# Kernel tuning notes

Hardware: AMD Instinct MI355X
Metric: run time of the kernel (lower is better)

Reference implementation:

```python
import jax, jax.numpy as jnp
import numpy as np

N = 16384
E = 524288
IN_DIM, H1, H2 = 256, 128, 64


def setup_inputs() -> dict:
    key = jax.random.key(0)
    ks = jax.random.split(key, 9)
    features = jax.random.normal(ks[0], (N, IN_DIM), dtype=jnp.float32)
    src = jax.random.randint(ks[1], (E,), 0, N, dtype=jnp.int32)
    dst = jax.random.randint(ks[2], (E,), 0, N, dtype=jnp.int32)
    s = 0.1
    W1 = jax.random.normal(ks[3], (IN_DIM, H1), dtype=jnp.float32) * s
    b1 = jnp.zeros((H1,), dtype=jnp.float32)
    W2 = jax.random.normal(ks[4], (H1, H1), dtype=jnp.float32) * s
    b2 = jnp.zeros((H1,), dtype=jnp.float32)
    W3 = jax.random.normal(ks[5], (H1, H2), dtype=jnp.float32) * s
    b3 = jnp.zeros((H2,), dtype=jnp.float32)
    return {"features": features, "src": src, "dst": dst,
            "W1": W1, "b1": b1, "W2": W2, "b2": b2, "W3": W3, "b3": b3}


def _degree_norms(src, dst):
    ones = jnp.ones(src.shape[0], dtype=jnp.float32)
    deg_out = jax.ops.segment_sum(ones, src, num_segments=N)
    deg_in = jax.ops.segment_sum(ones, dst, num_segments=N)
    # allow_zero_in_degree=True with norm='both': clamp degree to min 1
    norm_out = jax.lax.rsqrt(jnp.maximum(deg_out, 1.0))  # [N]
    norm_in = jax.lax.rsqrt(jnp.maximum(deg_in, 1.0))    # [N]
    return norm_out, norm_in


def _graph_conv(h, src, dst, norm_out, norm_in, W, b, relu):
    # DGL GraphConv, norm='both': D_in^{-1/2} A^T (D_out^{-1/2} h) W + b
    h = h * norm_out[:, None]
    msg = h[src]                                   # gather [E, d]
    agg = jax.ops.segment_sum(msg, dst, num_segments=N)  # scatter-add [N, d]
    out = agg * norm_in[:, None] @ W + b
    return jax.nn.relu(out) if relu else out


def reference(features, src, dst, W1, b1, W2, b2, W3, b3):
    norm_out, norm_in = _degree_norms(src, dst)
    h = _graph_conv(features, src, dst, norm_out, norm_in, W1, b1, True)
    h = _graph_conv(h, src, dst, norm_out, norm_in, W2, b2, True)
    z = _graph_conv(h, src, dst, norm_out, norm_in, W3, b3, False)  # [N, H2]
    adj_rec = jax.nn.sigmoid(z @ z.T)  # [N, N]
    return adj_rec, z
```

## Files before the change

kernel.cpp:

```cpp
#include <hip/hip_runtime.h>
#include <hip/hip_bf16.h>

#define NN 16384
#define EE 524288

constexpr int D0 = 256, D1 = 128, D2 = 64;

typedef __attribute__((ext_vector_type(8))) short short8;
typedef __attribute__((ext_vector_type(4))) float f32x4;

__device__ __forceinline__ float b2f(ushort u) {
  union { unsigned int i; float f; } x;
  x.i = ((unsigned int)u) << 16;
  return x.f;
}
__device__ __forceinline__ ushort f2b(float f) {
  __hip_bfloat16 h = __float2bfloat16(f);
  return *reinterpret_cast<ushort*>(&h);
}


__global__ __launch_bounds__(256) void count_deg_kernel(
    const int* __restrict__ src, const int* __restrict__ dst,
    int* __restrict__ deg_out, int* __restrict__ deg_in) {
  int e = blockIdx.x * 256 + threadIdx.x;
  if (e < EE) {
    atomicAdd(&deg_out[src[e]], 1);
    atomicAdd(&deg_in[dst[e]], 1);
  }
}

__global__ __launch_bounds__(256) void norm_kernel(
    const int* __restrict__ deg_out, const int* __restrict__ deg_in,
    float* __restrict__ norm_out, float* __restrict__ norm_in) {
  int i = blockIdx.x * 256 + threadIdx.x;
  if (i < NN) {
    norm_out[i] = rsqrtf(fmaxf((float)deg_out[i], 1.0f));
    norm_in[i]  = rsqrtf(fmaxf((float)deg_in[i], 1.0f));
  }
}

__global__ __launch_bounds__(256) void prefix_kernel(
    const int* __restrict__ deg_in, int* __restrict__ row_ptr,
    int* __restrict__ cursor) {
  __shared__ int part[256];
  int t = threadIdx.x;
  int base = t * 64;
  int s = 0;
  for (int j = 0; j < 64; ++j) s += deg_in[base + j];
  part[t] = s;
  __syncthreads();
  for (int off = 1; off < 256; off <<= 1) {
    int add = (t >= off) ? part[t - off] : 0;
    __syncthreads();
    part[t] += add;
    __syncthreads();
  }
  int run = (t == 0) ? 0 : part[t - 1];
  for (int j = 0; j < 64; ++j) {
    row_ptr[base + j] = run;
    cursor[base + j] = run;
    run += deg_in[base + j];
  }
  if (t == 255) row_ptr[NN] = run;
}

__global__ __launch_bounds__(256) void fill_csr_kernel(
    const int* __restrict__ src, const int* __restrict__ dst,
    int* __restrict__ cursor, int* __restrict__ csr_src) {
  int e = blockIdx.x * 256 + threadIdx.x;
  if (e < EE) {
    int pos = atomicAdd(&cursor[dst[e]], 1);
    csr_src[pos] = src[e];
  }
}


template<int DIN, int DOUT, int KC, bool OBF16>
__global__ __launch_bounds__(256) void gemm_kernel(
    const float* __restrict__ h, const float* __restrict__ W,
    const float* __restrict__ norm_out, float* __restrict__ tf,
    ushort* __restrict__ tb) {
  constexpr int W4 = DOUT / 4;
  constexpr int RG = 256 / W4;
  constexpr int RPT = 32 / RG;
  __shared__ float A[32][DIN];
  __shared__ float WC[KC][DOUT];
  int tid = threadIdx.x;
  int r0 = blockIdx.x * 32;
  constexpr int NF4 = 32 * DIN / 4;
  for (int q = tid; q < NF4; q += 256) {
    int r = q / (DIN / 4);
    int c = q % (DIN / 4);
    float4 x = *(const float4*)&h[(size_t)(r0 + r) * DIN + c * 4];
    float no = norm_out[r0 + r];
    x.x *= no; x.y *= no; x.z *= no; x.w *= no;
    *(float4*)&A[r][c * 4] = x;
  }
  int c4 = tid % W4;
  int rg = tid / W4;
  float4 acc[RPT];
#pragma unroll
  for (int j = 0; j < RPT; ++j) acc[j] = make_float4(0.f, 0.f, 0.f, 0.f);

  for (int kc = 0; kc < DIN / KC; ++kc) {
    __syncthreads();
#pragma unroll
    for (int q = 0; q < KC * W4 / 256; ++q)
      ((float4*)WC)[q * 256 + tid] =
          ((const float4*)W)[(size_t)kc * KC * W4 + q * 256 + tid];
    __syncthreads();
#pragma unroll 4
    for (int k2 = 0; k2 < KC; ++k2) {
      float4 w = *(const float4*)&WC[k2][c4 * 4];
#pragma unroll
      for (int j = 0; j < RPT; ++j) {
        float a = A[rg + j * RG][kc * KC + k2];
        acc[j].x += a * w.x; acc[j].y += a * w.y;
        acc[j].z += a * w.z; acc[j].w += a * w.w;
      }
    }
  }
#pragma unroll
  for (int j = 0; j < RPT; ++j) {
    size_t row = (size_t)(r0 + rg + j * RG);
    if (OBF16) {
      ushort4 o;
      o.x = f2b(acc[j].x); o.y = f2b(acc[j].y);
      o.z = f2b(acc[j].z); o.w = f2b(acc[j].w);
      *(ushort4*)&tb[row * DOUT + c4 * 4] = o;
    } else {
      *(float4*)&tf[row * DOUT + c4 * 4] = acc[j];
    }
  }
}


template<int DOUT, bool RELU>
__global__ __launch_bounds__(256) void gather_bf16_kernel(
    const ushort* __restrict__ t, const float* __restrict__ bias,
    const float* __restrict__ norm_in, const int* __restrict__ row_ptr,
    const int* __restrict__ csr, float* __restrict__ out) {
  constexpr int G8 = DOUT / 8;
  constexpr int S = 256 / G8;
  __shared__ float red[S][G8][8];
  int tid = threadIdx.x;
  int c8 = tid % G8, slot = tid / G8;
  int v = blockIdx.x;
  int k0 = row_ptr[v], k1 = row_ptr[v + 1];
  float a[8];
#pragma unroll
  for (int i = 0; i < 8; ++i) a[i] = 0.f;
  for (int k = k0 + slot; k < k1; k += S) {
    int s = csr[k];
    short8 m = *(const short8*)&t[(size_t)s * DOUT + c8 * 8];
#pragma unroll
    for (int i = 0; i < 8; ++i) a[i] += b2f((ushort)m[i]);
  }
#pragma unroll
  for (int i = 0; i < 8; ++i) red[slot][c8][i] = a[i];
  __syncthreads();
#pragma unroll
  for (int s = S / 2; s >= 1; s >>= 1) {
    if (slot < s) {
#pragma unroll
      for (int i = 0; i < 8; ++i) red[slot][c8][i] += red[slot + s][c8][i];
    }
    __syncthreads();
  }
  if (tid < G8) {
    float ni = norm_in[v];
    float o[8];
#pragma unroll
    for (int i = 0; i < 8; ++i) {
      o[i] = red[0][tid][i] * ni + bias[tid * 8 + i];
      if (RELU) o[i] = fmaxf(o[i], 0.f);
    }
    *(float4*)&out[(size_t)v * DOUT + tid * 8] = make_float4(o[0], o[1], o[2], o[3]);
    *(float4*)&out[(size_t)v * DOUT + tid * 8 + 4] = make_float4(o[4], o[5], o[6], o[7]);
  }
}


template<int DOUT, bool RELU>
__global__ __launch_bounds__(256) void gather_f32_kernel(
    const float* __restrict__ t, const float* __restrict__ bias,
    const float* __restrict__ norm_in, const int* __restrict__ row_ptr,
    const int* __restrict__ csr, float* __restrict__ out,
    ushort* __restrict__ zb) {
  constexpr int W4 = DOUT / 4;
  constexpr int S = 256 / W4;
  __shared__ float4 red[256];
  int tid = threadIdx.x;
  int c4 = tid % W4, slot = tid / W4;
  int v = blockIdx.x;
  int k0 = row_ptr[v], k1 = row_ptr[v + 1];
  float4 acc = make_float4(0.f, 0.f, 0.f, 0.f);
  for (int k = k0 + slot; k < k1; k += S) {
    int s = csr[k];
    float4 m = *(const float4*)&t[(size_t)s * DOUT + c4 * 4];
    acc.x += m.x; acc.y += m.y; acc.z += m.z; acc.w += m.w;
  }
  red[tid] = acc;
  __syncthreads();
  if (tid < W4) {
    float4 a = red[tid];
#pragma unroll
    for (int s = 1; s < S; ++s) {
      float4 b = red[s * W4 + tid];
      a.x += b.x; a.y += b.y; a.z += b.z; a.w += b.w;
    }
    float ni = norm_in[v];
    float4 b4 = *(const float4*)&bias[tid * 4];
    a.x = a.x * ni + b4.x; a.y = a.y * ni + b4.y;
    a.z = a.z * ni + b4.z; a.w = a.w * ni + b4.w;
    if (RELU) {
      a.x = fmaxf(a.x, 0.f); a.y = fmaxf(a.y, 0.f);
      a.z = fmaxf(a.z, 0.f); a.w = fmaxf(a.w, 0.f);
    }
    *(float4*)&out[(size_t)v * DOUT + tid * 4] = a;
    ushort4 ob;
    ob.x = f2b(a.x); ob.y = f2b(a.y); ob.z = f2b(a.z); ob.w = f2b(a.w);
    *(ushort4*)&zb[(size_t)v * DOUT + tid * 4] = ob;
  }
}


__global__ __launch_bounds__(256) void adj_mfma_kernel(
    const ushort* __restrict__ zb, float* __restrict__ C) {
  __shared__ ushort SMEM[2 * 128 * 64];
  ushort* ZR = SMEM;
  ushort* ZC = SMEM + 128 * 64;
  int t = threadIdx.x;
  int bx = blockIdx.x & 127, by = blockIdx.x >> 7;
  int row0 = by * 128, col0 = bx * 128;
  {
    int r = t >> 1;
    int ub = (t & 1) * 4;
    const float4* zr = (const float4*)(zb + (size_t)(row0 + r) * 64);
    const float4* zc = (const float4*)(zb + (size_t)(col0 + r) * 64);
    float4* LR = (float4*)ZR;
    float4* LC = (float4*)ZC;
#pragma unroll
    for (int u = 0; u < 4; ++u) {
      int sw = (ub + u) ^ (r & 7);
      LR[r * 8 + sw] = zr[ub + u];
      LC[r * 8 + sw] = zc[ub + u];
    }
  }
  __syncthreads();
  int l = t & 63, w = t >> 6;
  int wy = w >> 1, wx = w & 1;
  int lr = l & 15, lg = l >> 4;
  f32x4 acc[4][4];
#pragma unroll
  for (int i = 0; i < 4; ++i)
#pragma unroll
    for (int j = 0; j < 4; ++j) acc[i][j] = (f32x4){0.f, 0.f, 0.f, 0.f};

#pragma unroll
  for (int ks = 0; ks < 2; ++ks) {
    short8 af[4], bf_[4];
    int u = ks * 4 + lg;
#pragma unroll
    for (int i = 0; i < 4; ++i) {
      int ar = wy * 64 + i * 16 + lr;
      af[i] = *(const short8*)&ZR[ar * 64 + ((u ^ (ar & 7)) << 3)];
      int ac = wx * 64 + i * 16 + lr;
      bf_[i] = *(const short8*)&ZC[ac * 64 + ((u ^ (ac & 7)) << 3)];
    }
#pragma unroll
    for (int i = 0; i < 4; ++i)
#pragma unroll
      for (int j = 0; j < 4; ++j)
        acc[i][j] = __builtin_amdgcn_mfma_f32_16x16x32_bf16(
            bf_[j], af[i], acc[i][j], 0, 0, 0);
  }

  __syncthreads();
  float* scr = ((float*)SMEM) + w * (16 * 68);
  int sr = l >> 4;
  int sc = (l & 15) * 4;
  float* Cbase = C + (size_t)(row0 + wy * 64) * NN + col0 + wx * 64 + sc;
#pragma unroll
  for (int i = 0; i < 4; ++i) {
#pragma unroll
    for (int j = 0; j < 4; ++j) {
      f32x4 o;
      o[0] = __builtin_amdgcn_rcpf(1.0f + __expf(-acc[i][j][0]));
      o[1] = __builtin_amdgcn_rcpf(1.0f + __expf(-acc[i][j][1]));
      o[2] = __builtin_amdgcn_rcpf(1.0f + __expf(-acc[i][j][2]));
      o[3] = __builtin_amdgcn_rcpf(1.0f + __expf(-acc[i][j][3]));
      *(f32x4*)&scr[lr * 68 + j * 16 + lg * 4] = o;
    }
    __syncthreads();
#pragma unroll
    for (int rp = 0; rp < 4; ++rp) {
      int rloc = rp * 4 + sr;
      float4 v = *(const float4*)&scr[rloc * 68 + sc];
      *(float4*)&Cbase[(size_t)(i * 16 + rloc) * NN] = v;
    }
    __syncthreads();
  }
}


extern "C" void kernel_launch(void* const* d_in, const int* in_sizes, int n_in,
                              void* d_out, int out_size, void* d_ws, size_t ws_size,
                              hipStream_t stream) {
  const float* features = (const float*)d_in[0];
  const int* src = (const int*)d_in[1];
  const int* dst = (const int*)d_in[2];
  const float* W1 = (const float*)d_in[3];
  const float* b1 = (const float*)d_in[4];
  const float* W2 = (const float*)d_in[5];
  const float* b2 = (const float*)d_in[6];
  const float* W3 = (const float*)d_in[7];
  const float* b3 = (const float*)d_in[8];

  float* outp = (float*)d_out;
  float* adj = outp;
  float* z = outp + (size_t)NN * NN;

  ushort* tb = (ushort*)adj;
  float* hbuf = adj + (size_t)NN * 64;
  float* t3 = adj + (size_t)NN * 192;

  float* wsf = (float*)d_ws;
  float* norm_out = wsf;
  float* norm_in = wsf + NN;
  int* deg_out = (int*)(wsf + 2 * NN);
  int* deg_in = deg_out + NN;
  int* row_ptr = deg_in + NN;
  int* cursor = row_ptr + NN + 256;
  int* csr_src = cursor + NN;
  ushort* zb = (ushort*)(csr_src + EE);

  hipMemsetAsync(deg_out, 0, 2 * NN * sizeof(int), stream);
  count_deg_kernel<<<EE / 256, 256, 0, stream>>>(src, dst, deg_out, deg_in);
  norm_kernel<<<NN / 256, 256, 0, stream>>>(deg_out, deg_in, norm_out, norm_in);
  prefix_kernel<<<1, 256, 0, stream>>>(deg_in, row_ptr, cursor);
  fill_csr_kernel<<<EE / 256, 256, 0, stream>>>(src, dst, cursor, csr_src);

  gemm_kernel<D0, D1, 32, true><<<NN / 32, 256, 0, stream>>>(
      features, W1, norm_out, nullptr, tb);
  gather_bf16_kernel<D1, true><<<NN, 256, 0, stream>>>(
      tb, b1, norm_in, row_ptr, csr_src, hbuf);
  gemm_kernel<D1, D1, 64, true><<<NN / 32, 256, 0, stream>>>(
      hbuf, W2, norm_out, nullptr, tb);
  gather_bf16_kernel<D1, true><<<NN, 256, 0, stream>>>(
      tb, b2, norm_in, row_ptr, csr_src, hbuf);
  gemm_kernel<D1, D2, 64, false><<<NN / 32, 256, 0, stream>>>(
      hbuf, W3, norm_out, t3, nullptr);
  gather_f32_kernel<D2, false><<<NN, 256, 0, stream>>>(
      t3, b3, norm_in, row_ptr, csr_src, z, zb);

  adj_mfma_kernel<<<(NN / 128) * (NN / 128), 256, 0, stream>>>(zb, adj);
}
```

Measured before the change: 399.3 us.

## Replace per-node gather kernels with edge-balanced multi-node segmented gather

Replaces the one-block-per-node gather kernels with a single templated kernel that handles 16 destination nodes per block. The block's edge range is split evenly across thread lanes, and partial sums are flushed into shared-memory accumulators with atomics at node boundaries. This targets the launch and reduction overhead of 16K tiny blocks and the load imbalance between nodes of different degree. The cost is shared-memory atomics and extra boundary-tracking logic in the inner loop.

New measurement: 426.9 us. 1.07x slower.

```diff
diff --git a/kernel.cpp b/kernel.cpp
--- a/kernel.cpp
+++ b/kernel.cpp
@@ -136,92 +136,87 @@
 }
 
 
-template<int DOUT, bool RELU>
-__global__ __launch_bounds__(256) void gather_bf16_kernel(
-    const ushort* __restrict__ t, const float* __restrict__ bias,
-    const float* __restrict__ norm_in, const int* __restrict__ row_ptr,
-    const int* __restrict__ csr, float* __restrict__ out) {
-  constexpr int G8 = DOUT / 8;
-  constexpr int S = 256 / G8;
-  __shared__ float red[S][G8][8];
-  int tid = threadIdx.x;
-  int c8 = tid % G8, slot = tid / G8;
-  int v = blockIdx.x;
-  int k0 = row_ptr[v], k1 = row_ptr[v + 1];
-  float a[8];
-#pragma unroll
-  for (int i = 0; i < 8; ++i) a[i] = 0.f;
-  for (int k = k0 + slot; k < k1; k += S) {
-    int s = csr[k];
-    short8 m = *(const short8*)&t[(size_t)s * DOUT + c8 * 8];
-#pragma unroll
-    for (int i = 0; i < 8; ++i) a[i] += b2f((ushort)m[i]);
-  }
-#pragma unroll
-  for (int i = 0; i < 8; ++i) red[slot][c8][i] = a[i];
-  __syncthreads();
-#pragma unroll
-  for (int s = S / 2; s >= 1; s >>= 1) {
-    if (slot < s) {
-#pragma unroll
-      for (int i = 0; i < 8; ++i) red[slot][c8][i] += red[slot + s][c8][i];
-    }
-    __syncthreads();
-  }
-  if (tid < G8) {
-    float ni = norm_in[v];
-    float o[8];
-#pragma unroll
-    for (int i = 0; i < 8; ++i) {
-      o[i] = red[0][tid][i] * ni + bias[tid * 8 + i];
-      if (RELU) o[i] = fmaxf(o[i], 0.f);
-    }
-    *(float4*)&out[(size_t)v * DOUT + tid * 8] = make_float4(o[0], o[1], o[2], o[3]);
-    *(float4*)&out[(size_t)v * DOUT + tid * 8 + 4] = make_float4(o[4], o[5], o[6], o[7]);
-  }
-}
-
-
-template<int DOUT, bool RELU>
-__global__ __launch_bounds__(256) void gather_f32_kernel(
-    const float* __restrict__ t, const float* __restrict__ bias,
+template<int DOUT, int NPB, bool RELU, bool BF16IN, bool WRITEZB>
+__global__ __launch_bounds__(256) void gather_seg_kernel(
+    const void* __restrict__ tptr, const float* __restrict__ bias,
     const float* __restrict__ norm_in, const int* __restrict__ row_ptr,
     const int* __restrict__ csr, float* __restrict__ out,
     ushort* __restrict__ zb) {
-  constexpr int W4 = DOUT / 4;
-  constexpr int S = 256 / W4;
-  __shared__ float4 red[256];
+  constexpr int CG = DOUT / 8;
+  constexpr int EL = 256 / CG;
+  __shared__ float acc[NPB][DOUT];
+  __shared__ int rp[NPB + 1];
   int tid = threadIdx.x;
-  int c4 = tid % W4, slot = tid / W4;
-  int v = blockIdx.x;
-  int k0 = row_ptr[v], k1 = row_ptr[v + 1];
-  float4 acc = make_float4(0.f, 0.f, 0.f, 0.f);
-  for (int k = k0 + slot; k < k1; k += S) {
-    int s = csr[k];
-    float4 m = *(const float4*)&t[(size_t)s * DOUT + c4 * 4];
-    acc.x += m.x; acc.y += m.y; acc.z += m.z; acc.w += m.w;
-  }
-  red[tid] = acc;
-  __syncthreads();
-  if (tid < W4) {
-    float4 a = red[tid];
-#pragma unroll
-    for (int s = 1; s < S; ++s) {
-      float4 b = red[s * W4 + tid];
-      a.x += b.x; a.y += b.y; a.z += b.z; a.w += b.w;
-    }
-    float ni = norm_in[v];
-    float4 b4 = *(const float4*)&bias[tid * 4];
-    a.x = a.x * ni + b4.x; a.y = a.y * ni + b4.y;
-    a.z = a.z * ni + b4.z; a.w = a.w * ni + b4.w;
+  int v0 = blockIdx.x * NPB;
+  if (tid <= NPB) rp[tid] = row_ptr[v0 + tid];
+  for (int q = tid; q < NPB * DOUT; q += 256) ((float*)acc)[q] = 0.f;
+  __syncthreads();
+
+  int cg = tid % CG;
+  int el = tid / CG;
+  int e0 = rp[0], e1 = rp[NPB];
+  int cnt = e1 - e0;
+  int chunk = (cnt + EL - 1) / EL;
+  int s = e0 + el * chunk;
+  int e = min(s + chunk, e1);
+
+  int d = 0;
+  while (d < NPB - 1 && rp[d + 1] <= s) ++d;
+
+  float a[8];
+#pragma unroll
+  for (int i = 0; i < 8; ++i) a[i] = 0.f;
+  bool dirty = false;
+
+  for (int k = s; k < e; ++k) {
+    if (k >= rp[d + 1]) {
+      if (dirty) {
+#pragma unroll
+        for (int i = 0; i < 8; ++i) atomicAdd(&acc[d][cg * 8 + i], a[i]);
+#pragma unroll
+        for (int i = 0; i < 8; ++i) a[i] = 0.f;
+        dirty = false;
+      }
+      do { ++d; } while (d < NPB - 1 && rp[d + 1] <= k);
+    }
+    int srcn = csr[k];
+    if (BF16IN) {
+      short8 m = *(const short8*)((const ushort*)tptr + (size_t)srcn * DOUT + cg * 8);
+#pragma unroll
+      for (int i = 0; i < 8; ++i) a[i] += b2f((ushort)m[i]);
+    } else {
+      const float* tf = (const float*)tptr + (size_t)srcn * DOUT + cg * 8;
+      float4 m0 = *(const float4*)tf;
+      float4 m1 = *(const float4*)(tf + 4);
+      a[0] += m0.x; a[1] += m0.y; a[2] += m0.z; a[3] += m0.w;
+      a[4] += m1.x; a[5] += m1.y; a[6] += m1.z; a[7] += m1.w;
+    }
+    dirty = true;
+  }
+  if (dirty) {
+#pragma unroll
+    for (int i = 0; i < 8; ++i) atomicAdd(&acc[d][cg * 8 + i], a[i]);
+  }
+  __syncthreads();
+
+  constexpr int R4 = DOUT / 4;
+  for (int q = tid; q < NPB * R4; q += 256) {
+    int n = q / R4, c = q % R4;
+    float4 x = *(const float4*)&acc[n][c * 4];
+    float ni = norm_in[v0 + n];
+    float4 b4 = *(const float4*)&bias[c * 4];
+    x.x = x.x * ni + b4.x; x.y = x.y * ni + b4.y;
+    x.z = x.z * ni + b4.z; x.w = x.w * ni + b4.w;
     if (RELU) {
-      a.x = fmaxf(a.x, 0.f); a.y = fmaxf(a.y, 0.f);
-      a.z = fmaxf(a.z, 0.f); a.w = fmaxf(a.w, 0.f);
-    }
-    *(float4*)&out[(size_t)v * DOUT + tid * 4] = a;
-    ushort4 ob;
-    ob.x = f2b(a.x); ob.y = f2b(a.y); ob.z = f2b(a.z); ob.w = f2b(a.w);
-    *(ushort4*)&zb[(size_t)v * DOUT + tid * 4] = ob;
+      x.x = fmaxf(x.x, 0.f); x.y = fmaxf(x.y, 0.f);
+      x.z = fmaxf(x.z, 0.f); x.w = fmaxf(x.w, 0.f);
+    }
+    *(float4*)&out[(size_t)(v0 + n) * DOUT + c * 4] = x;
+    if (WRITEZB) {
+      ushort4 ob;
+      ob.x = f2b(x.x); ob.y = f2b(x.y); ob.z = f2b(x.z); ob.w = f2b(x.w);
+      *(ushort4*)&zb[(size_t)(v0 + n) * DOUT + c * 4] = ob;
+    }
   }
 }
 
@@ -344,15 +339,15 @@
 
   gemm_kernel<D0, D1, 32, true><<<NN / 32, 256, 0, stream>>>(
       features, W1, norm_out, nullptr, tb);
-  gather_bf16_kernel<D1, true><<<NN, 256, 0, stream>>>(
-      tb, b1, norm_in, row_ptr, csr_src, hbuf);
+  gather_seg_kernel<D1, 16, true, true, false><<<NN / 16, 256, 0, stream>>>(
+      tb, b1, norm_in, row_ptr, csr_src, hbuf, nullptr);
   gemm_kernel<D1, D1, 64, true><<<NN / 32, 256, 0, stream>>>(
       hbuf, W2, norm_out, nullptr, tb);
-  gather_bf16_kernel<D1, true><<<NN, 256, 0, stream>>>(
-      tb, b2, norm_in, row_ptr, csr_src, hbuf);
+  gather_seg_kernel<D1, 16, true, true, false><<<NN / 16, 256, 0, stream>>>(
+      tb, b2, norm_in, row_ptr, csr_src, hbuf, nullptr);
   gemm_kernel<D1, D2, 64, false><<<NN / 32, 256, 0, stream>>>(
       hbuf, W3, norm_out, t3, nullptr);
-  gather_f32_kernel<D2, false><<<NN, 256, 0, stream>>>(
+  gather_seg_kernel<D2, 16, false, false, true><<<NN / 16, 256, 0, stream>>>(
       t3, b3, norm_in, row_ptr, csr_src, z, zb);
 
   adj_mfma_kernel<<<(NN / 128) * (NN / 128), 256, 0, stream>>>(zb, adj);
```

## Store hidden activations in bf16, fuse norm into scan, stage CSR in LDS

Applied to the files above, without the earlier changes.

Hidden activations between layers and the layer-3 transform are now stored as bf16 instead of fp32. The GEMM converts them on load, and a single gather kernel template writes bf16 output plus optional fp32 z. The norm and prefix kernels merge into one 1024-thread scan kernel, removing a launch. The gather kernel stages up to 256 CSR indices in LDS and issues two neighbour loads per iteration. Together these cut memory traffic and launch count, but the extra bf16 rounding of the intermediates lowers accuracy.

Result: no change. 399.7 us (+0.1%).

```diff
diff --git a/kernel.cpp b/kernel.cpp
--- a/kernel.cpp
+++ b/kernel.cpp
@@ -30,39 +30,35 @@
   }
 }
 
-__global__ __launch_bounds__(256) void norm_kernel(
-    const int* __restrict__ deg_out, const int* __restrict__ deg_in,
+__global__ __launch_bounds__(1024) void scan_all_kernel(
+    const int* __restrict__ deg_in, const int* __restrict__ deg_out,
+    int* __restrict__ row_ptr, int* __restrict__ cursor,
     float* __restrict__ norm_out, float* __restrict__ norm_in) {
-  int i = blockIdx.x * 256 + threadIdx.x;
-  if (i < NN) {
-    norm_out[i] = rsqrtf(fmaxf((float)deg_out[i], 1.0f));
-    norm_in[i]  = rsqrtf(fmaxf((float)deg_in[i], 1.0f));
-  }
-}
-
-__global__ __launch_bounds__(256) void prefix_kernel(
-    const int* __restrict__ deg_in, int* __restrict__ row_ptr,
-    int* __restrict__ cursor) {
-  __shared__ int part[256];
+  __shared__ int part[1024];
   int t = threadIdx.x;
-  int base = t * 64;
+  int base = t * 16;
+  int loc[16];
   int s = 0;
-  for (int j = 0; j < 64; ++j) s += deg_in[base + j];
+#pragma unroll
+  for (int j = 0; j < 16; ++j) { loc[j] = deg_in[base + j]; s += loc[j]; }
   part[t] = s;
   __syncthreads();
-  for (int off = 1; off < 256; off <<= 1) {
+  for (int off = 1; off < 1024; off <<= 1) {
     int add = (t >= off) ? part[t - off] : 0;
     __syncthreads();
     part[t] += add;
     __syncthreads();
   }
   int run = (t == 0) ? 0 : part[t - 1];
-  for (int j = 0; j < 64; ++j) {
+#pragma unroll
+  for (int j = 0; j < 16; ++j) {
     row_ptr[base + j] = run;
     cursor[base + j] = run;
-    run += deg_in[base + j];
-  }
-  if (t == 255) row_ptr[NN] = run;
+    norm_in[base + j] = rsqrtf(fmaxf((float)loc[j], 1.0f));
+    norm_out[base + j] = rsqrtf(fmaxf((float)deg_out[base + j], 1.0f));
+    run += loc[j];
+  }
+  if (t == 1023) row_ptr[NN] = run;
 }
 
 __global__ __launch_bounds__(256) void fill_csr_kernel(
@@ -76,11 +72,10 @@
 }
 
 
-template<int DIN, int DOUT, int KC, bool OBF16>
+template<int DIN, int DOUT, int KC, bool INBF16>
 __global__ __launch_bounds__(256) void gemm_kernel(
-    const float* __restrict__ h, const float* __restrict__ W,
-    const float* __restrict__ norm_out, float* __restrict__ tf,
-    ushort* __restrict__ tb) {
+    const void* __restrict__ hp, const float* __restrict__ W,
+    const float* __restrict__ norm_out, ushort* __restrict__ tb) {
   constexpr int W4 = DOUT / 4;
   constexpr int RG = 256 / W4;
   constexpr int RPT = 32 / RG;
@@ -88,14 +83,26 @@
   __shared__ float WC[KC][DOUT];
   int tid = threadIdx.x;
   int r0 = blockIdx.x * 32;
-  constexpr int NF4 = 32 * DIN / 4;
-  for (int q = tid; q < NF4; q += 256) {
-    int r = q / (DIN / 4);
-    int c = q % (DIN / 4);
-    float4 x = *(const float4*)&h[(size_t)(r0 + r) * DIN + c * 4];
-    float no = norm_out[r0 + r];
-    x.x *= no; x.y *= no; x.z *= no; x.w *= no;
-    *(float4*)&A[r][c * 4] = x;
+  if (INBF16) {
+    constexpr int NF8 = 32 * DIN / 8;
+    for (int q = tid; q < NF8; q += 256) {
+      int r = q / (DIN / 8);
+      int c = q % (DIN / 8);
+      short8 m = *(const short8*)((const ushort*)hp + (size_t)(r0 + r) * DIN + c * 8);
+      float no = norm_out[r0 + r];
+#pragma unroll
+      for (int i = 0; i < 8; ++i) A[r][c * 8 + i] = b2f((ushort)m[i]) * no;
+    }
+  } else {
+    constexpr int NF4 = 32 * DIN / 4;
+    for (int q = tid; q < NF4; q += 256) {
+      int r = q / (DIN / 4);
+      int c = q % (DIN / 4);
+      float4 x = *(const float4*)((const float*)hp + (size_t)(r0 + r) * DIN + c * 4);
+      float no = norm_out[r0 + r];
+      x.x *= no; x.y *= no; x.z *= no; x.w *= no;
+      *(float4*)&A[r][c * 4] = x;
+    }
   }
   int c4 = tid % W4;
   int rg = tid / W4;
@@ -124,38 +131,47 @@
 #pragma unroll
   for (int j = 0; j < RPT; ++j) {
     size_t row = (size_t)(r0 + rg + j * RG);
-    if (OBF16) {
-      ushort4 o;
-      o.x = f2b(acc[j].x); o.y = f2b(acc[j].y);
-      o.z = f2b(acc[j].z); o.w = f2b(acc[j].w);
-      *(ushort4*)&tb[row * DOUT + c4 * 4] = o;
-    } else {
-      *(float4*)&tf[row * DOUT + c4 * 4] = acc[j];
-    }
-  }
-}
-
-
-template<int DOUT, bool RELU>
-__global__ __launch_bounds__(256) void gather_bf16_kernel(
+    ushort4 o;
+    o.x = f2b(acc[j].x); o.y = f2b(acc[j].y);
+    o.z = f2b(acc[j].z); o.w = f2b(acc[j].w);
+    *(ushort4*)&tb[row * DOUT + c4 * 4] = o;
+  }
+}
+
+
+template<int DOUT, bool RELU, bool WRITEZ>
+__global__ __launch_bounds__(256) void gather_kernel(
     const ushort* __restrict__ t, const float* __restrict__ bias,
     const float* __restrict__ norm_in, const int* __restrict__ row_ptr,
-    const int* __restrict__ csr, float* __restrict__ out) {
+    const int* __restrict__ csr, ushort* __restrict__ outb,
+    float* __restrict__ zout) {
   constexpr int G8 = DOUT / 8;
   constexpr int S = 256 / G8;
   __shared__ float red[S][G8][8];
+  __shared__ int ecsr[256];
   int tid = threadIdx.x;
   int c8 = tid % G8, slot = tid / G8;
   int v = blockIdx.x;
   int k0 = row_ptr[v], k1 = row_ptr[v + 1];
+  int nk = k1 - k0;
+  if (tid < nk && tid < 256) ecsr[tid] = csr[k0 + tid];
+  __syncthreads();
   float a[8];
 #pragma unroll
   for (int i = 0; i < 8; ++i) a[i] = 0.f;
-  for (int k = k0 + slot; k < k1; k += S) {
-    int s = csr[k];
-    short8 m = *(const short8*)&t[(size_t)s * DOUT + c8 * 8];
-#pragma unroll
-    for (int i = 0; i < 8; ++i) a[i] += b2f((ushort)m[i]);
+  for (int k = slot; k < nk; k += 2 * S) {
+    int s0 = (k < 256) ? ecsr[k] : csr[k0 + k];
+    int kb = k + S;
+    bool h2 = kb < nk;
+    int s1 = h2 ? ((kb < 256) ? ecsr[kb] : csr[k0 + kb]) : s0;
+    short8 m0 = *(const short8*)&t[(size_t)s0 * DOUT + c8 * 8];
+    short8 m1 = *(const short8*)&t[(size_t)s1 * DOUT + c8 * 8];
+#pragma unroll
+    for (int i = 0; i < 8; ++i) a[i] += b2f((ushort)m0[i]);
+    if (h2) {
+#pragma unroll
+      for (int i = 0; i < 8; ++i) a[i] += b2f((ushort)m1[i]);
+    }
   }
 #pragma unroll
   for (int i = 0; i < 8; ++i) red[slot][c8][i] = a[i];
@@ -176,52 +192,17 @@
       o[i] = red[0][tid][i] * ni + bias[tid * 8 + i];
       if (RELU) o[i] = fmaxf(o[i], 0.f);
     }
-    *(float4*)&out[(size_t)v * DOUT + tid * 8] = make_float4(o[0], o[1], o[2], o[3]);
-    *(float4*)&out[(size_t)v * DOUT + tid * 8 + 4] = make_float4(o[4], o[5], o[6], o[7]);
-  }
-}
-
-
-template<int DOUT, bool RELU>
-__global__ __launch_bounds__(256) void gather_f32_kernel(
-    const float* __restrict__ t, const float* __restrict__ bias,
-    const float* __restrict__ norm_in, const int* __restrict__ row_ptr,
-    const int* __restrict__ csr, float* __restrict__ out,
-    ushort* __restrict__ zb) {
-  constexpr int W4 = DOUT / 4;
-  constexpr int S = 256 / W4;
-  __shared__ float4 red[256];
-  int tid = threadIdx.x;
-  int c4 = tid % W4, slot = tid / W4;
-  int v = blockIdx.x;
-  int k0 = row_ptr[v], k1 = row_ptr[v + 1];
-  float4 acc = make_float4(0.f, 0.f, 0.f, 0.f);
-  for (int k = k0 + slot; k < k1; k += S) {
-    int s = csr[k];
-    float4 m = *(const float4*)&t[(size_t)s * DOUT + c4 * 4];
-    acc.x += m.x; acc.y += m.y; acc.z += m.z; acc.w += m.w;
-  }
-  red[tid] = acc;
-  __syncthreads();
-  if (tid < W4) {
-    float4 a = red[tid];
-#pragma unroll
-    for (int s = 1; s < S; ++s) {
-      float4 b = red[s * W4 + tid];
-      a.x += b.x; a.y += b.y; a.z += b.z; a.w += b.w;
-    }
-    float ni = norm_in[v];
-    float4 b4 = *(const float4*)&bias[tid * 4];
-    a.x = a.x * ni + b4.x; a.y = a.y * ni + b4.y;
-    a.z = a.z * ni + b4.z; a.w = a.w * ni + b4.w;
-    if (RELU) {
-      a.x = fmaxf(a.x, 0.f); a.y = fmaxf(a.y, 0.f);
-      a.z = fmaxf(a.z, 0.f); a.w = fmaxf(a.w, 0.f);
-    }
-    *(float4*)&out[(size_t)v * DOUT + tid * 4] = a;
-    ushort4 ob;
-    ob.x = f2b(a.x); ob.y = f2b(a.y); ob.z = f2b(a.z); ob.w = f2b(a.w);
-    *(ushort4*)&zb[(size_t)v * DOUT + tid * 4] = ob;
+    ushort4 b0, b1;
+    b0.x = f2b(o[0]); b0.y = f2b(o[1]); b0.z = f2b(o[2]); b0.w = f2b(o[3]);
+    b1.x = f2b(o[4]); b1.y = f2b(o[5]); b1.z = f2b(o[6]); b1.w = f2b(o[7]);
+    ushort* op = outb + (size_t)v * DOUT + tid * 8;
+    *(ushort4*)op = b0;
+    *(ushort4*)(op + 4) = b1;
+    if (WRITEZ) {
+      float* zp = zout + (size_t)v * DOUT + tid * 8;
+      *(float4*)zp = make_float4(o[0], o[1], o[2], o[3]);
+      *(float4*)(zp + 4) = make_float4(o[4], o[5], o[6], o[7]);
+    }
   }
 }
 
@@ -323,8 +304,7 @@
   float* z = outp + (size_t)NN * NN;
 
   ushort* tb = (ushort*)adj;
-  float* hbuf = adj + (size_t)NN * 64;
-  float* t3 = adj + (size_t)NN * 192;
+  ushort* hb = (ushort*)(adj + (size_t)NN * 64);
 
   float* wsf = (float*)d_ws;
   float* norm_out = wsf;
@@ -338,22 +318,22 @@
 
   hipMemsetAsync(deg_out, 0, 2 * NN * sizeof(int), stream);
   count_deg_kernel<<<EE / 256, 256, 0, stream>>>(src, dst, deg_out, deg_in);
-  norm_kernel<<<NN / 256, 256, 0, stream>>>(deg_out, deg_in, norm_out, norm_in);
-  prefix_kernel<<<1, 256, 0, stream>>>(deg_in, row_ptr, cursor);
+  scan_all_kernel<<<1, 1024, 0, stream>>>(deg_in, deg_out, row_ptr, cursor,
+                                          norm_out, norm_in);
   fill_csr_kernel<<<EE / 256, 256, 0, stream>>>(src, dst, cursor, csr_src);
 
-  gemm_kernel<D0, D1, 32, true><<<NN / 32, 256, 0, stream>>>(
-      features, W1, norm_out, nullptr, tb);
-  gather_bf16_kernel<D1, true><<<NN, 256, 0, stream>>>(
-      tb, b1, norm_in, row_ptr, csr_src, hbuf);
+  gemm_kernel<D0, D1, 32, false><<<NN / 32, 256, 0, stream>>>(
+      features, W1, norm_out, tb);
+  gather_kernel<D1, true, false><<<NN, 256, 0, stream>>>(
+      tb, b1, norm_in, row_ptr, csr_src, hb, nullptr);
   gemm_kernel<D1, D1, 64, true><<<NN / 32, 256, 0, stream>>>(
-      hbuf, W2, norm_out, nullptr, tb);
-  gather_bf16_kernel<D1, true><<<NN, 256, 0, stream>>>(
-      tb, b2, norm_in, row_ptr, csr_src, hbuf);
-  gemm_kernel<D1, D2, 64, false><<<NN / 32, 256, 0, stream>>>(
-      hbuf, W3, norm_out, t3, nullptr);
-  gather_f32_kernel<D2, false><<<NN, 256, 0, stream>>>(
-      t3, b3, norm_in, row_ptr, csr_src, z, zb);
+      hb, W2, norm_out, tb);
+  gather_kernel<D1, true, false><<<NN, 256, 0, stream>>>(
+      tb, b2, norm_in, row_ptr, csr_src, hb, nullptr);
+  gemm_kernel<D1, D2, 64, true><<<NN / 32, 256, 0, stream>>>(
+      hb, W3, norm_out, tb);
+  gather_kernel<D2, false, true><<<NN, 256, 0, stream>>>(
+      tb, b3, norm_in, row_ptr, csr_src, zb, z);
 
   adj_mfma_kernel<<<(NN / 128) * (NN / 128), 256, 0, stream>>>(zb, adj);
 }
```
